# Kernel optimization log

Measured on AMD Instinct MI355X. Metric: run time of the kernel, lower is better.

## Reference

```python
import jax, jax.numpy as jnp
import numpy as np

IN_FEATURES = 2048
OUT_FEATURES = 8192


def ternary_quantize(w):
    # BitNet 1.58b: scale = mean(|w|), round to {-1,0,1}, rescale
    scale = jnp.mean(jnp.abs(w)) + 1e-8
    w_q = jnp.clip(jnp.round(w / scale), -1.0, 1.0)
    return w_q * scale


def setup_inputs() -> dict:
    key = jax.random.key(0)
    kx, kw = jax.random.split(key)
    x = jax.random.normal(kx, (4, 2048, IN_FEATURES), dtype=jnp.float32)
    # nn.init.normal_(std=1/sqrt(in_features))
    weight = jax.random.normal(kw, (OUT_FEATURES, IN_FEATURES), dtype=jnp.float32) / np.sqrt(IN_FEATURES)
    return {"x": x, "weight": weight}


def reference(x, weight):
    w = ternary_quantize(weight)
    # F.linear: x @ w.T  -> [B, S, out_features]
    return jnp.einsum('bsd,od->bso', x, w)
```

## Files before the change

### kernel.cpp

```cpp
#include <hip/hip_runtime.h>
#include <hip/hip_bf16.h>
#include <stdint.h>


typedef __attribute__((ext_vector_type(8))) short   s16x8;
typedef __attribute__((ext_vector_type(4))) float   f32x4;

#define K_DIM   2048
#define K2      4096
#define N_DIM   8192
#define N4      4194304

__global__ void k_abs_part(const float4* __restrict__ w4, float* __restrict__ part) {
    int tid = blockIdx.x * 256 + threadIdx.x;
    float s = 0.f;
    for (int i = tid; i < N4; i += gridDim.x * 256) {
        float4 v = w4[i];
        s += fabsf(v.x) + fabsf(v.y) + fabsf(v.z) + fabsf(v.w);
    }
    for (int off = 32; off > 0; off >>= 1) s += __shfl_down(s, off, 64);
    __shared__ float tmp[4];
    int lane = threadIdx.x & 63, wid = threadIdx.x >> 6;
    if (lane == 0) tmp[wid] = s;
    __syncthreads();
    if (threadIdx.x == 0) part[blockIdx.x] = tmp[0] + tmp[1] + tmp[2] + tmp[3];
}

__global__ void k_abs_final(const float* __restrict__ part, float* __restrict__ scale) {
    float s = part[threadIdx.x] + part[threadIdx.x + 256] +
              part[threadIdx.x + 512] + part[threadIdx.x + 768];
    for (int off = 32; off > 0; off >>= 1) s += __shfl_down(s, off, 64);
    __shared__ float tmp[4];
    int lane = threadIdx.x & 63, wid = threadIdx.x >> 6;
    if (lane == 0) tmp[wid] = s;
    __syncthreads();
    if (threadIdx.x == 0) scale[0] = (tmp[0] + tmp[1] + tmp[2] + tmp[3]) / 16777216.0f + 1e-8f;
}

__device__ __forceinline__ uint32_t f2b(float f) {
    uint32_t u = __builtin_bit_cast(uint32_t, f);
    return (u + 0x7FFFu + ((u >> 16) & 1u)) >> 16;
}

__global__ void k_prep(const float4* __restrict__ w4, const float4* __restrict__ x4,
                       const float* __restrict__ scale_p,
                       uint2* __restrict__ wq, uint2* __restrict__ xb) {
    int tid = (blockIdx.x & 2047) * 256 + threadIdx.x;
    if (blockIdx.x < 2048) {
        const float sc = *scale_p;
        for (int i = tid; i < N4; i += 2048 * 256) {
            float4 v = w4[i];
            float q0 = rintf(v.x / sc), q1 = rintf(v.y / sc);
            float q2 = rintf(v.z / sc), q3 = rintf(v.w / sc);
            uint32_t b0 = (q0 == 0.f) ? 0u : (q0 > 0.f ? 0x3F80u : 0xBF80u);
            uint32_t b1 = (q1 == 0.f) ? 0u : (q1 > 0.f ? 0x3F80u : 0xBF80u);
            uint32_t b2 = (q2 == 0.f) ? 0u : (q2 > 0.f ? 0x3F80u : 0xBF80u);
            uint32_t b3 = (q3 == 0.f) ? 0u : (q3 > 0.f ? 0x3F80u : 0xBF80u);
            uint2 o; o.x = b0 | (b1 << 16); o.y = b2 | (b3 << 16);
            wq[i] = o;
        }
    } else {
        for (int i = tid; i < N4; i += 2048 * 256) {
            float4 v = x4[i];
            uint2 o;
            o.x = f2b(v.x) | (f2b(v.y) << 16);
            o.y = f2b(v.z) | (f2b(v.w) << 16);
            xb[i] = o;
        }
    }
}

__device__ __forceinline__ void mfma16(f32x4& c, s16x8 a, s16x8 b) {
    asm("v_mfma_f32_16x16x32_bf16 %0, %1, %2, %0" : "+v"(c) : "v"(a), "v"(b));
}
__device__ __forceinline__ void load_lds16(const void* g, void* l) {
    __builtin_amdgcn_global_load_lds(
        (const __attribute__((address_space(1))) uint32_t*)g,
        (__attribute__((address_space(3))) uint32_t*)l, 16, 0, 0);
}

#define SBAR do { __builtin_amdgcn_sched_barrier(0); __builtin_amdgcn_s_barrier(); \
                  __builtin_amdgcn_sched_barrier(0); } while (0)
#define LGKM0 do { asm volatile("s_waitcnt lgkmcnt(0)" ::: "memory"); \
                   __builtin_amdgcn_sched_barrier(0); } while (0)
#define WAIT_VM(N) do { asm volatile("s_waitcnt vmcnt(" #N ")" ::: "memory"); \
                        __builtin_amdgcn_sched_barrier(0); } while (0)

#define A0_BASE 0
#define B0_BASE 32768
#define A1_BASE 65536
#define B1_BASE 98304

__global__ __launch_bounds__(512, 2) void k_gemm(
    const unsigned short* __restrict__ Xb,
    const unsigned short* __restrict__ Wb,
    const float* __restrict__ scale_p,
    float* __restrict__ out)
{
    extern __shared__ uint8_t smem[];
    const int tid  = threadIdx.x;
    const int lane = tid & 63;
    const int wid  = tid >> 6;
    const int wr   = wid >> 2;
    const int wc   = wid & 3;

    const int bid = blockIdx.x;
    const int swz = (bid & 7) * 128 + (bid >> 3);
    const int tileRow = swz >> 5;
    const int tileCol = swz & 31;

    const uint8_t* gA = (const uint8_t*)Xb + (size_t)tileRow * 256 * K2;
    const uint8_t* gB = (const uint8_t*)Wb + (size_t)tileCol * 256 * K2;

    const int srow = tid >> 3, sslot = tid & 7;
    const size_t srcOff = (size_t)srow * K2 + (size_t)((sslot ^ (srow & 7)) * 16);
    const uint8_t* gAs = gA + srcOff;
    const uint8_t* gBs = gB + srcOff;
    const int dstOff = tid * 16;

    const int rA = wr * 128 + (lane & 15);
    const int rB = wc * 64  + (lane & 15);
    const int h  = lane >> 4;
    const int pA0 = rA * 128 + (((h    ) ^ (rA & 7)) * 16);
    const int pA1 = rA * 128 + (((4 + h) ^ (rA & 7)) * 16);
    const int pB0 = rB * 128 + (((h    ) ^ (rB & 7)) * 16);
    const int pB1 = rB * 128 + (((4 + h) ^ (rB & 7)) * 16);

    s16x8 a[8][2], b[4][2];
    f32x4 acc[8][4];
    #pragma unroll
    for (int m = 0; m < 8; ++m)
        #pragma unroll
        for (int n = 0; n < 4; ++n) acc[m][n] = (f32x4){0.f, 0.f, 0.f, 0.f};

#define LD8(OFF) (*(const s16x8*)(smem + (OFF)))
#define STAGE(LBASE, GP, BOFF) do { \
    load_lds16((GP) + (BOFF),          smem + (LBASE) + dstOff); \
    load_lds16((GP) + (BOFF) + 262144, smem + (LBASE) + 8192 + dstOff); } while (0)

#define READS_FIRST(ABASE) do { \
    _Pragma("unroll") for (int m = 0; m < 4; ++m) { \
        a[m][0] = LD8((ABASE) + pA0 + m * 2048); \
        a[m][1] = LD8((ABASE) + pA1 + m * 2048); } \
    _Pragma("unroll") for (int n = 0; n < 2; ++n) { \
        b[n][0] = LD8((ABASE) + 32768 + pB0 + n * 2048); \
        b[n][1] = LD8((ABASE) + 32768 + pB1 + n * 2048); } } while (0)

#define READS_SECOND(ABASE) do { \
    _Pragma("unroll") for (int n = 2; n < 4; ++n) { \
        b[n][0] = LD8((ABASE) + 32768 + pB0 + n * 2048); \
        b[n][1] = LD8((ABASE) + 32768 + pB1 + n * 2048); } \
    _Pragma("unroll") for (int m = 4; m < 8; ++m) { \
        a[m][0] = LD8((ABASE) + pA0 + m * 2048); \
        a[m][1] = LD8((ABASE) + pA1 + m * 2048); } } while (0)

#define MFMA_Q(MLO, NLO) do { \
    __builtin_amdgcn_s_setprio(1); \
    _Pragma("unroll") for (int kk = 0; kk < 2; ++kk) \
        _Pragma("unroll") for (int m = 0; m < 4; ++m) \
            _Pragma("unroll") for (int n = 0; n < 2; ++n) \
                mfma16(acc[(MLO) + m][(NLO) + n], a[(MLO) + m][kk], b[(NLO) + n][kk]); \
    __builtin_amdgcn_s_setprio(0); \
    __builtin_amdgcn_sched_barrier(0); } while (0)

    STAGE(A0_BASE,         gAs, 0);
    STAGE(A0_BASE + 16384, gAs, 524288);
    STAGE(B0_BASE,         gBs, 0);
    STAGE(B0_BASE + 16384, gBs, 524288);
    STAGE(A1_BASE,         gAs, 128);
    STAGE(A1_BASE + 16384, gAs, 524288 + 128);
    WAIT_VM(4);
    SBAR;

    #pragma unroll 1
    for (int i = 0; i < 15; ++i) {
        const int kb1 = (2 * i + 1) * 128;
        const int kb2 = kb1 + 128;
        const int kb3 = kb1 + 256;
        READS_FIRST(A0_BASE);
        STAGE(B1_BASE, gBs, kb1);
        SBAR; LGKM0; MFMA_Q(0, 0); SBAR;
        READS_SECOND(A0_BASE);
        STAGE(B1_BASE + 16384, gBs, 524288 + kb1);
        SBAR; LGKM0; MFMA_Q(0, 2); SBAR;
        STAGE(A0_BASE, gAs, kb2);
        SBAR; MFMA_Q(4, 0); SBAR;
        STAGE(A0_BASE + 16384, gAs, 524288 + kb2);
        SBAR; MFMA_Q(4, 2); WAIT_VM(4); SBAR;
        READS_FIRST(A1_BASE);
        STAGE(B0_BASE, gBs, kb2);
        SBAR; LGKM0; MFMA_Q(0, 0); SBAR;
        READS_SECOND(A1_BASE);
        STAGE(B0_BASE + 16384, gBs, 524288 + kb2);
        SBAR; LGKM0; MFMA_Q(0, 2); SBAR;
        STAGE(A1_BASE, gAs, kb3);
        SBAR; MFMA_Q(4, 0); SBAR;
        STAGE(A1_BASE + 16384, gAs, 524288 + kb3);
        SBAR; MFMA_Q(4, 2); WAIT_VM(4); SBAR;
    }

    READS_FIRST(A0_BASE);
    STAGE(B1_BASE, gBs, 31 * 128);
    SBAR; LGKM0; MFMA_Q(0, 0); SBAR;
    READS_SECOND(A0_BASE);
    STAGE(B1_BASE + 16384, gBs, 524288 + 31 * 128);
    SBAR; LGKM0; MFMA_Q(0, 2); SBAR;
    MFMA_Q(4, 0);
    MFMA_Q(4, 2);
    WAIT_VM(0); SBAR;
    READS_FIRST(A1_BASE);
    SBAR; LGKM0; MFMA_Q(0, 0); SBAR;
    READS_SECOND(A1_BASE);
    SBAR; LGKM0; MFMA_Q(0, 2); SBAR;
    MFMA_Q(4, 0);
    MFMA_Q(4, 2);

    const float sc = *scale_p;
    const int orow0 = tileRow * 256 + wr * 128 + ((lane >> 4) << 2);
    const int ocol0 = tileCol * 256 + wc * 64 + (lane & 15);
    #pragma unroll
    for (int m = 0; m < 8; ++m)
        #pragma unroll
        for (int n = 0; n < 4; ++n)
            #pragma unroll
            for (int j = 0; j < 4; ++j)
                out[(size_t)(orow0 + m * 16 + j) * N_DIM + (ocol0 + n * 16)] = acc[m][n][j] * sc;

#undef LD8
#undef STAGE
#undef READS_FIRST
#undef READS_SECOND
#undef MFMA_Q
}

extern "C" void kernel_launch(void* const* d_in, const int* in_sizes, int n_in,
                              void* d_out, int out_size, void* d_ws, size_t ws_size,
                              hipStream_t stream) {
    const float* x = (const float*)d_in[0];
    const float* w = (const float*)d_in[1];
    float* out = (float*)d_out;
    uint8_t* ws = (uint8_t*)d_ws;

    float* part  = (float*)ws;
    float* scale = (float*)(ws + 4096);
    unsigned short* Xb = (unsigned short*)(ws + 8192);
    unsigned short* Wb = (unsigned short*)(ws + 8192 + 33554432ull);

    (void)hipFuncSetAttribute((const void*)k_gemm,
                              hipFuncAttributeMaxDynamicSharedMemorySize, 131072);

    hipLaunchKernelGGL(k_abs_part, dim3(1024), dim3(256), 0, stream, (const float4*)w, part);
    hipLaunchKernelGGL(k_abs_final, dim3(1), dim3(256), 0, stream, part, scale);
    hipLaunchKernelGGL(k_prep, dim3(4096), dim3(256), 0, stream,
                       (const float4*)w, (const float4*)x, scale, (uint2*)Wb, (uint2*)Xb);
    hipLaunchKernelGGL(k_gemm, dim3(1024), dim3(512), 131072, stream, Xb, Wb, scale, out);
}
```

Before: 329.4 us.

## Restructure GEMM main loop into two-buffer A+B pipeline with one barrier per tile

Reorganizes the LDS layout so each stage buffer holds both A and B for one K tile, and prefetches the next tile's first register fragments during the current tile's last MFMA quadrants. The number of workgroup barriers per K tile drops from eight to one, and LDS reads for the next tile overlap with compute. In exchange, each tile waits on all outstanding global loads (vmcnt(0)) before its single barrier, so global-load latency hiding shrinks to about one tile ahead.

```diff
diff --git a/kernel.cpp b/kernel.cpp
--- a/kernel.cpp
+++ b/kernel.cpp
@@ -79,17 +79,13 @@
         (__attribute__((address_space(3))) uint32_t*)l, 16, 0, 0);
 }
 
-#define SBAR do { __builtin_amdgcn_sched_barrier(0); __builtin_amdgcn_s_barrier(); \
-                  __builtin_amdgcn_sched_barrier(0); } while (0)
-#define LGKM0 do { asm volatile("s_waitcnt lgkmcnt(0)" ::: "memory"); \
-                   __builtin_amdgcn_sched_barrier(0); } while (0)
-#define WAIT_VM(N) do { asm volatile("s_waitcnt vmcnt(" #N ")" ::: "memory"); \
-                        __builtin_amdgcn_sched_barrier(0); } while (0)
+#define SCHED0 __builtin_amdgcn_sched_barrier(0)
+#define SBAR do { SCHED0; __builtin_amdgcn_s_barrier(); SCHED0; } while (0)
+#define LGKM0 do { asm volatile("s_waitcnt lgkmcnt(0)" ::: "memory"); SCHED0; } while (0)
+#define WAIT_VM(N) do { asm volatile("s_waitcnt vmcnt(" #N ")" ::: "memory"); SCHED0; } while (0)
 
 #define A0_BASE 0
-#define B0_BASE 32768
 #define A1_BASE 65536
-#define B1_BASE 98304
 
 __global__ __launch_bounds__(512, 2) void k_gemm(
     const unsigned short* __restrict__ Xb,
@@ -138,21 +134,14 @@
     load_lds16((GP) + (BOFF),          smem + (LBASE) + dstOff); \
     load_lds16((GP) + (BOFF) + 262144, smem + (LBASE) + 8192 + dstOff); } while (0)
 
-#define READS_FIRST(ABASE) do { \
-    _Pragma("unroll") for (int m = 0; m < 4; ++m) { \
-        a[m][0] = LD8((ABASE) + pA0 + m * 2048); \
-        a[m][1] = LD8((ABASE) + pA1 + m * 2048); } \
-    _Pragma("unroll") for (int n = 0; n < 2; ++n) { \
-        b[n][0] = LD8((ABASE) + 32768 + pB0 + n * 2048); \
-        b[n][1] = LD8((ABASE) + 32768 + pB1 + n * 2048); } } while (0)
-
-#define READS_SECOND(ABASE) do { \
-    _Pragma("unroll") for (int n = 2; n < 4; ++n) { \
-        b[n][0] = LD8((ABASE) + 32768 + pB0 + n * 2048); \
-        b[n][1] = LD8((ABASE) + 32768 + pB1 + n * 2048); } \
-    _Pragma("unroll") for (int m = 4; m < 8; ++m) { \
-        a[m][0] = LD8((ABASE) + pA0 + m * 2048); \
-        a[m][1] = LD8((ABASE) + pA1 + m * 2048); } } while (0)
+#define RD_A03(AB) do { _Pragma("unroll") for (int m = 0; m < 4; ++m) { \
+    a[m][0] = LD8((AB) + pA0 + m * 2048); a[m][1] = LD8((AB) + pA1 + m * 2048); } } while (0)
+#define RD_A47(AB) do { _Pragma("unroll") for (int m = 4; m < 8; ++m) { \
+    a[m][0] = LD8((AB) + pA0 + m * 2048); a[m][1] = LD8((AB) + pA1 + m * 2048); } } while (0)
+#define RD_B01(AB) do { _Pragma("unroll") for (int n = 0; n < 2; ++n) { \
+    b[n][0] = LD8((AB) + 32768 + pB0 + n * 2048); b[n][1] = LD8((AB) + 32768 + pB1 + n * 2048); } } while (0)
+#define RD_B23(AB) do { _Pragma("unroll") for (int n = 2; n < 4; ++n) { \
+    b[n][0] = LD8((AB) + 32768 + pB0 + n * 2048); b[n][1] = LD8((AB) + 32768 + pB1 + n * 2048); } } while (0)
 
 #define MFMA_Q(MLO, NLO) do { \
     __builtin_amdgcn_s_setprio(1); \
@@ -161,59 +150,51 @@
             _Pragma("unroll") for (int n = 0; n < 2; ++n) \
                 mfma16(acc[(MLO) + m][(NLO) + n], a[(MLO) + m][kk], b[(NLO) + n][kk]); \
     __builtin_amdgcn_s_setprio(0); \
-    __builtin_amdgcn_sched_barrier(0); } while (0)
+    SCHED0; } while (0)
+
+#define TILE(CURA, NXTA, KB2, SEN, NEN) do { \
+     \
+    RD_B23(CURA); SCHED0; \
+    MFMA_Q(0, 0); \
+     \
+    RD_A47(CURA); SCHED0; \
+    MFMA_Q(0, 2); \
+     \
+    LGKM0; WAIT_VM(0); SBAR; \
+    if (SEN) { STAGE((CURA), gAs, (KB2)); STAGE((CURA) + 16384, gAs, 524288 + (KB2)); } \
+    if (NEN) RD_A03(NXTA); \
+    SCHED0; \
+    MFMA_Q(4, 0); \
+     \
+    if (SEN) { STAGE((CURA) + 32768, gBs, (KB2)); STAGE((CURA) + 49152, gBs, 524288 + (KB2)); } \
+    if (NEN) RD_B01(NXTA); \
+    SCHED0; \
+    MFMA_Q(4, 2); \
+} while (0)
 
     STAGE(A0_BASE,         gAs, 0);
     STAGE(A0_BASE + 16384, gAs, 524288);
-    STAGE(B0_BASE,         gBs, 0);
-    STAGE(B0_BASE + 16384, gBs, 524288);
+    STAGE(A0_BASE + 32768, gBs, 0);
+    STAGE(A0_BASE + 49152, gBs, 524288);
     STAGE(A1_BASE,         gAs, 128);
     STAGE(A1_BASE + 16384, gAs, 524288 + 128);
-    WAIT_VM(4);
+    STAGE(A1_BASE + 32768, gBs, 128);
+    STAGE(A1_BASE + 49152, gBs, 524288 + 128);
+    WAIT_VM(8);
     SBAR;
+    RD_A03(A0_BASE);
+    RD_B01(A0_BASE);
+    SCHED0;
 
     #pragma unroll 1
     for (int i = 0; i < 15; ++i) {
-        const int kb1 = (2 * i + 1) * 128;
-        const int kb2 = kb1 + 128;
-        const int kb3 = kb1 + 256;
-        READS_FIRST(A0_BASE);
-        STAGE(B1_BASE, gBs, kb1);
-        SBAR; LGKM0; MFMA_Q(0, 0); SBAR;
-        READS_SECOND(A0_BASE);
-        STAGE(B1_BASE + 16384, gBs, 524288 + kb1);
-        SBAR; LGKM0; MFMA_Q(0, 2); SBAR;
-        STAGE(A0_BASE, gAs, kb2);
-        SBAR; MFMA_Q(4, 0); SBAR;
-        STAGE(A0_BASE + 16384, gAs, 524288 + kb2);
-        SBAR; MFMA_Q(4, 2); WAIT_VM(4); SBAR;
-        READS_FIRST(A1_BASE);
-        STAGE(B0_BASE, gBs, kb2);
-        SBAR; LGKM0; MFMA_Q(0, 0); SBAR;
-        READS_SECOND(A1_BASE);
-        STAGE(B0_BASE + 16384, gBs, 524288 + kb2);
-        SBAR; LGKM0; MFMA_Q(0, 2); SBAR;
-        STAGE(A1_BASE, gAs, kb3);
-        SBAR; MFMA_Q(4, 0); SBAR;
-        STAGE(A1_BASE + 16384, gAs, 524288 + kb3);
-        SBAR; MFMA_Q(4, 2); WAIT_VM(4); SBAR;
+        const int kb0 = (2 * i + 2) * 128;
+        const int kb1 = (2 * i + 3) * 128;
+        TILE(A0_BASE, A1_BASE, kb0, 1, 1);
+        TILE(A1_BASE, A0_BASE, kb1, 1, 1);
     }
-
-    READS_FIRST(A0_BASE);
-    STAGE(B1_BASE, gBs, 31 * 128);
-    SBAR; LGKM0; MFMA_Q(0, 0); SBAR;
-    READS_SECOND(A0_BASE);
-    STAGE(B1_BASE + 16384, gBs, 524288 + 31 * 128);
-    SBAR; LGKM0; MFMA_Q(0, 2); SBAR;
-    MFMA_Q(4, 0);
-    MFMA_Q(4, 2);
-    WAIT_VM(0); SBAR;
-    READS_FIRST(A1_BASE);
-    SBAR; LGKM0; MFMA_Q(0, 0); SBAR;
-    READS_SECOND(A1_BASE);
-    SBAR; LGKM0; MFMA_Q(0, 2); SBAR;
-    MFMA_Q(4, 0);
-    MFMA_Q(4, 2);
+    TILE(A0_BASE, A1_BASE, 0, 0, 1);
+    TILE(A1_BASE, A0_BASE, 0, 0, 0);
 
     const float sc = *scale_p;
     const int orow0 = tileRow * 256 + wr * 128 + ((lane >> 4) << 2);
@@ -228,9 +209,12 @@
 
 #undef LD8
 #undef STAGE
-#undef READS_FIRST
-#undef READS_SECOND
+#undef RD_A03
+#undef RD_A47
+#undef RD_B01
+#undef RD_B23
 #undef MFMA_Q
+#undef TILE
 }
 
 extern "C" void kernel_launch(void* const* d_in, const int* in_sizes, int n_in,
```

New measurement: 372.9 us. 1.13x slower.
